# Performance work log

Measured on AMD Instinct MI355X. Metric: run time of the kernel, lower is better.

The kernel has to match this reference:

```python
import jax, jax.numpy as jnp
import numpy as np

C = 384
NUM_HEADS = 6
HEAD_SIZE = C // NUM_HEADS
EPS = 1e-5


def setup_inputs() -> dict:
    key = jax.random.key(0)
    ks = jax.random.split(key, 16)
    sc = lambda *s: 0.02
    inp = {
        'x': jax.random.normal(ks[0], (256, 256, C), dtype=jnp.float32),
        'Wq': jax.random.normal(ks[1], (NUM_HEADS, C, HEAD_SIZE), dtype=jnp.float32) * 0.02,
        'Wk': jax.random.normal(ks[2], (NUM_HEADS, C, HEAD_SIZE), dtype=jnp.float32) * 0.02,
        'Wv': jax.random.normal(ks[3], (NUM_HEADS, C, HEAD_SIZE), dtype=jnp.float32) * 0.02,
        'Wp': jax.random.normal(ks[4], (C, C), dtype=jnp.float32) * 0.02,
        'bp': jnp.zeros((C,), dtype=jnp.float32),
        'W1': jax.random.normal(ks[5], (C, 4 * C), dtype=jnp.float32) * 0.02,
        'b1': jnp.zeros((4 * C,), dtype=jnp.float32),
        'W2': jax.random.normal(ks[6], (4 * C, C), dtype=jnp.float32) * 0.02,
        'b2': jnp.zeros((C,), dtype=jnp.float32),
        'g1': jnp.ones((C,), dtype=jnp.float32),
        'be1': jnp.zeros((C,), dtype=jnp.float32),
        'g2': jnp.ones((C,), dtype=jnp.float32),
        'be2': jnp.zeros((C,), dtype=jnp.float32),
    }
    return inp


def _layernorm(x, g, b):
    mu = jnp.mean(x, axis=-1, keepdims=True)
    var = jnp.mean(jnp.square(x - mu), axis=-1, keepdims=True)
    return (x - mu) * jax.lax.rsqrt(var + EPS) * g + b


def reference(x, Wq, Wk, Wv, Wp, bp, W1, b1, W2, b2, g1, be1, g2, be2):
    B, T, _ = x.shape
    # --- attention sublayer (dropout = identity in eval) ---
    h = _layernorm(x, g1, be1)
    Q = jnp.einsum('btc,hcd->bhtd', h, Wq)
    K = jnp.einsum('btc,hcd->bhtd', h, Wk)
    V = jnp.einsum('btc,hcd->bhtd', h, Wv)
    scores = jnp.einsum('bhtd,bhsd->bhts', Q, K) / jnp.sqrt(jnp.float32(HEAD_SIZE))
    causal = jnp.tril(jnp.ones((T, T), dtype=bool))
    scores = jnp.where(causal, scores, -jnp.inf)
    attn = jax.nn.softmax(scores, axis=-1)
    out = jnp.einsum('bhts,bhsd->bhtd', attn, V)  # [B,H,T,d]
    out = out.transpose(0, 2, 1, 3).reshape(B, T, C)  # concat heads
    x = x + out @ Wp + bp
    # --- feed-forward sublayer ---
    h2 = _layernorm(x, g2, be2)
    ff = jax.nn.relu(h2 @ W1 + b1) @ W2 + b2
    return x + ff
```

## Files before the change

### kernel.cpp

```cpp
#include <hip/hip_runtime.h>
#include <hip/hip_bf16.h>


typedef __attribute__((ext_vector_type(8))) short bf16x8;
typedef __attribute__((ext_vector_type(4))) float f32x4;
typedef unsigned short u16;
typedef unsigned int u32;

#define MFMA16(a, b, c) __builtin_amdgcn_mfma_f32_16x16x32_bf16((a), (b), (c), 0, 0, 0)

__device__ __forceinline__ void gl2lds16(const void* g, void* l) {
  __builtin_amdgcn_global_load_lds((const __attribute__((address_space(1))) u32*)g,
                                   (__attribute__((address_space(3))) u32*)l, 16, 0, 0);
}

__device__ __forceinline__ u16 f2bf(float f) {
  __hip_bfloat16 h = __float2bfloat16(f);
  return *(u16*)&h;
}
__device__ __forceinline__ float bf2f(u16 u) {
  __hip_bfloat16 h;
  *(u16*)&h = u;
  return __bfloat162float(h);
}

template <int HAS_BIAS, int HAS_RES, int RELU, int OUT_BF16>
__global__ __launch_bounds__(256) void gemm_bt(const u16* __restrict__ A,
                                               const u16* __restrict__ Bt,
                                               const float* __restrict__ bias,
                                               const float* res, void* outp,
                                               int M, int N, int K) {
  __shared__ __attribute__((aligned(16))) u16 As[128 * 32];
  __shared__ __attribute__((aligned(16))) u16 Bs[128 * 32];
  const int m0 = blockIdx.y * 128, n0 = blockIdx.x * 128;
  const int w = threadIdx.x >> 6, l = threadIdx.x & 63;
  const int lm = l & 15, quad = l >> 4;
  const int wm = (w >> 1) * 64, wn = (w & 1) * 64;
  f32x4 acc[4][4];
#pragma unroll
  for (int i = 0; i < 4; ++i)
#pragma unroll
    for (int j = 0; j < 4; ++j) acc[i][j] = 0.f;

  for (int k0 = 0; k0 < K; k0 += 32) {
#pragma unroll
    for (int j = 0; j < 2; ++j) {
      int ci = w * 128 + j * 64 + l;
      int row = ci >> 2, cc = ci & 3;
      gl2lds16(A + (size_t)(m0 + row) * K + k0 + cc * 8, &As[(w * 128 + j * 64) * 8]);
      gl2lds16(Bt + (size_t)(n0 + row) * K + k0 + cc * 8, &Bs[(w * 128 + j * 64) * 8]);
    }
    __syncthreads();
    bf16x8 af[4], bfb[4];
#pragma unroll
    for (int i = 0; i < 4; ++i)
      af[i] = *(const bf16x8*)&As[(wm + i * 16 + lm) * 32 + quad * 8];
#pragma unroll
    for (int j = 0; j < 4; ++j)
      bfb[j] = *(const bf16x8*)&Bs[(wn + j * 16 + lm) * 32 + quad * 8];
#pragma unroll
    for (int i = 0; i < 4; ++i)
#pragma unroll
      for (int j = 0; j < 4; ++j) acc[i][j] = MFMA16(af[i], bfb[j], acc[i][j]);
    __syncthreads();
  }
#pragma unroll
  for (int i = 0; i < 4; ++i) {
#pragma unroll
    for (int j = 0; j < 4; ++j) {
      int col = n0 + wn + j * 16 + lm;
      float bs = HAS_BIAS ? bias[col] : 0.f;
#pragma unroll
      for (int r = 0; r < 4; ++r) {
        int row = m0 + wm + i * 16 + quad * 4 + r;
        float v = acc[i][j][r] + bs;
        if (RELU) v = fmaxf(v, 0.f);
        if (HAS_RES) v += res[(size_t)row * N + col];
        if (OUT_BF16)
          ((u16*)outp)[(size_t)row * N + col] = f2bf(v);
        else
          ((float*)outp)[(size_t)row * N + col] = v;
      }
    }
  }
}

__global__ __launch_bounds__(256) void ln_kernel(const float* __restrict__ x,
                                                 const float* __restrict__ g,
                                                 const float* __restrict__ be,
                                                 u16* __restrict__ out) {
  int row = blockIdx.x * 4 + (threadIdx.x >> 6);
  int l = threadIdx.x & 63;
  const float* xr = x + (size_t)row * 384;
  float v[6];
  float s = 0.f;
#pragma unroll
  for (int i = 0; i < 6; ++i) {
    v[i] = xr[l + i * 64];
    s += v[i];
  }
#pragma unroll
  for (int o = 1; o < 64; o <<= 1) s += __shfl_xor(s, o, 64);
  float mu = s * (1.f / 384.f);
  float var = 0.f;
#pragma unroll
  for (int i = 0; i < 6; ++i) {
    float d = v[i] - mu;
    var += d * d;
  }
#pragma unroll
  for (int o = 1; o < 64; o <<= 1) var += __shfl_xor(var, o, 64);
  float rs = rsqrtf(var * (1.f / 384.f) + 1e-5f);
  u16* orow = out + (size_t)row * 384;
#pragma unroll
  for (int i = 0; i < 6; ++i)
    orow[l + i * 64] = f2bf((v[i] - mu) * rs * g[l + i * 64] + be[l + i * 64]);
}

__global__ void wT_kernel(const float* __restrict__ in, u16* __restrict__ out,
                          int K, int N) {
  int idx = blockIdx.x * 256 + threadIdx.x;
  if (idx >= K * N) return;
  int n = idx / K, k = idx - n * K;
  out[idx] = f2bf(in[(size_t)k * N + n]);
}

__global__ void qkvT_kernel(const float* __restrict__ W, u16* __restrict__ out) {
  int idx = blockIdx.x * 256 + threadIdx.x;
  if (idx >= 6 * 384 * 64) return;
  int r = idx / 384;
  int c = idx - r * 384;
  int h = r >> 6, d = r & 63;
  out[idx] = f2bf(W[(size_t)(h * 384 + c) * 64 + d]);
}

template <int TQ>
__global__ __launch_bounds__(256) void attn_kernel(const u16* __restrict__ qkv,
                                                   u16* __restrict__ attnout) {
  constexpr int NFULL = (TQ + 1) * 64;
  constexpr int NJ = NFULL / 16;
  constexpr int KSTEPS = NFULL / 32;
  int bh = blockIdx.x;
  int h = bh % 6, b = bh / 6;
  int tid = threadIdx.x;
  int w = tid >> 6, l = tid & 63;
  int lm = l & 15, quad = l >> 4;

  __shared__ __attribute__((aligned(16))) unsigned char smx[65536];
  u16* Qs = (u16*)smx;
  u16* Ks = (u16*)(smx + 9216);
  u16* P = (u16*)smx;
  u16* Vt = (u16*)(smx + 32768);

  const u16* Qg = qkv + ((size_t)(b * 256 + TQ * 64)) * 1152 + h * 64;
  const u16* Kg = qkv + ((size_t)(b * 256)) * 1152 + 384 + h * 64;
  const u16* Vg = qkv + ((size_t)(b * 256)) * 1152 + 768 + h * 64;

  for (int i = tid; i < 64 * 64; i += 256) {
    int r = i >> 6, d = i & 63;
    Qs[r * 72 + d] = f2bf(0.125f * bf2f(Qg[(size_t)r * 1152 + d]));
  }
  for (int i = tid; i < NFULL * 64; i += 256) {
    int r = i >> 6, d = i & 63;
    Ks[r * 72 + d] = Kg[(size_t)r * 1152 + d];
  }
  __syncthreads();

  f32x4 sacc[NJ];
#pragma unroll
  for (int jt = 0; jt < NJ; ++jt) sacc[jt] = 0.f;
#pragma unroll
  for (int kk = 0; kk < 2; ++kk) {
    bf16x8 aq = *(const bf16x8*)&Qs[(w * 16 + lm) * 72 + kk * 32 + quad * 8];
#pragma unroll
    for (int jt = 0; jt < NJ; ++jt) {
      bf16x8 bk = *(const bf16x8*)&Ks[(jt * 16 + lm) * 72 + kk * 32 + quad * 8];
      sacc[jt] = MFMA16(aq, bk, sacc[jt]);
    }
  }
  __syncthreads();

  int trow = TQ * 64 + w * 16 + quad * 4;
  float inv_l[4];
#pragma unroll
  for (int reg = 0; reg < 4; ++reg) {
    float m_ = -3.0e38f;
#pragma unroll
    for (int jt = 0; jt < NJ; ++jt) {
      int col = jt * 16 + lm;
      if (col <= trow + reg) m_ = fmaxf(m_, sacc[jt][reg]);
    }
#pragma unroll
    for (int o = 1; o < 16; o <<= 1) m_ = fmaxf(m_, __shfl_xor(m_, o, 16));
    float s_ = 0.f;
#pragma unroll
    for (int jt = 0; jt < NJ; ++jt) {
      int col = jt * 16 + lm;
      float p = (col <= trow + reg) ? __expf(sacc[jt][reg] - m_) : 0.f;
      sacc[jt][reg] = p;
      s_ += p;
    }
#pragma unroll
    for (int o = 1; o < 16; o <<= 1) s_ += __shfl_xor(s_, o, 16);
    inv_l[reg] = 1.f / s_;
  }
#pragma unroll
  for (int jt = 0; jt < NJ; ++jt) {
#pragma unroll
    for (int reg = 0; reg < 4; ++reg) {
      int m = w * 16 + quad * 4 + reg;
      int col = jt * 16 + lm;
      P[m * 256 + (col ^ ((m & 7) * 8))] = f2bf(sacc[jt][reg] * inv_l[reg]);
    }
  }
  for (int i = tid; i < NFULL * 64; i += 256) {
    int s = i >> 6, d = i & 63;
    Vt[d * 256 + (s ^ ((d & 7) * 8))] = Vg[(size_t)s * 1152 + d];
  }
  __syncthreads();

  f32x4 oacc[4];
#pragma unroll
  for (int jt = 0; jt < 4; ++jt) oacc[jt] = 0.f;
#pragma unroll
  for (int ks = 0; ks < KSTEPS; ++ks) {
    int m = w * 16 + lm;
    int kc = ks * 32 + quad * 8;
    bf16x8 ap = *(const bf16x8*)&P[m * 256 + (kc ^ ((m & 7) * 8))];
#pragma unroll
    for (int jt = 0; jt < 4; ++jt) {
      int n = jt * 16 + lm;
      bf16x8 bv = *(const bf16x8*)&Vt[n * 256 + (kc ^ ((n & 7) * 8))];
      oacc[jt] = MFMA16(ap, bv, oacc[jt]);
    }
  }
  u16* Og = attnout + ((size_t)(b * 256 + TQ * 64)) * 384 + h * 64;
#pragma unroll
  for (int jt = 0; jt < 4; ++jt)
#pragma unroll
    for (int r = 0; r < 4; ++r)
      Og[(size_t)(w * 16 + quad * 4 + r) * 384 + jt * 16 + lm] = f2bf(oacc[jt][r]);
}

extern "C" void kernel_launch(void* const* d_in, const int* in_sizes, int n_in,
                              void* d_out, int out_size, void* d_ws, size_t ws_size,
                              hipStream_t stream) {
  const float* x = (const float*)d_in[0];
  const float* Wq = (const float*)d_in[1];
  const float* Wk = (const float*)d_in[2];
  const float* Wv = (const float*)d_in[3];
  const float* Wp = (const float*)d_in[4];
  const float* bp = (const float*)d_in[5];
  const float* W1 = (const float*)d_in[6];
  const float* b1 = (const float*)d_in[7];
  const float* W2 = (const float*)d_in[8];
  const float* b2 = (const float*)d_in[9];
  const float* g1 = (const float*)d_in[10];
  const float* be1 = (const float*)d_in[11];
  const float* g2 = (const float*)d_in[12];
  const float* be2 = (const float*)d_in[13];
  float* out = (float*)d_out;

  const int BT = 65536;
  char* ws = (char*)d_ws;
  u16* qkv = (u16*)(ws);
  u16* attnout = (u16*)(ws + 150994944);
  u16* ff1 = (u16*)(ws);
  u16* h = (u16*)(ws + 201326592);
  u16* WqkvT = (u16*)(ws + 251658240);
  u16* WpT = (u16*)(ws + 252542976);
  u16* W1T = (u16*)(ws + 252837888);
  u16* W2T = (u16*)(ws + 254017536);

  qkvT_kernel<<<576, 256, 0, stream>>>(Wq, WqkvT);
  qkvT_kernel<<<576, 256, 0, stream>>>(Wk, WqkvT + 384 * 384);
  qkvT_kernel<<<576, 256, 0, stream>>>(Wv, WqkvT + 2 * 384 * 384);
  wT_kernel<<<576, 256, 0, stream>>>(Wp, WpT, 384, 384);
  wT_kernel<<<2304, 256, 0, stream>>>(W1, W1T, 384, 1536);
  wT_kernel<<<2304, 256, 0, stream>>>(W2, W2T, 1536, 384);

  ln_kernel<<<BT / 4, 256, 0, stream>>>(x, g1, be1, h);
  gemm_bt<0, 0, 0, 1><<<dim3(9, 512), 256, 0, stream>>>(h, WqkvT, nullptr, nullptr,
                                                        qkv, BT, 1152, 384);
  attn_kernel<0><<<1536, 256, 0, stream>>>(qkv, attnout);
  attn_kernel<1><<<1536, 256, 0, stream>>>(qkv, attnout);
  attn_kernel<2><<<1536, 256, 0, stream>>>(qkv, attnout);
  attn_kernel<3><<<1536, 256, 0, stream>>>(qkv, attnout);
  gemm_bt<1, 1, 0, 0><<<dim3(3, 512), 256, 0, stream>>>(attnout, WpT, bp, x, out,
                                                        BT, 384, 384);
  ln_kernel<<<BT / 4, 256, 0, stream>>>(out, g2, be2, h);
  gemm_bt<1, 0, 1, 1><<<dim3(12, 512), 256, 0, stream>>>(h, W1T, b1, nullptr, ff1,
                                                         BT, 1536, 384);
  gemm_bt<1, 1, 0, 0><<<dim3(3, 512), 256, 0, stream>>>(ff1, W2T, b2, out, out,
                                                        BT, 384, 1536);
}
```

Baseline: 905.9 us.

## Widen GEMM K-tile with swizzle, head-major QKV layout, fuse attention launches

The GEMM loads 64-wide K tiles into XOR-swizzled LDS and remaps block IDs so neighbouring M tiles stay on one XCD. The QKV projection writes a head-major layout, so attention can load Q, K and V with 16-byte vector loads. The Q scaling is folded into the softmax exponent, and the four attention launches become one grid. LayerNorm uses float2 loads and packed bf16 stores. The cost is larger LDS use per GEMM block and a scattered store pattern in the QKV epilogue.

```diff
diff --git a/kernel.cpp b/kernel.cpp
--- a/kernel.cpp
+++ b/kernel.cpp
@@ -23,16 +23,23 @@
   *(u16*)&h = u;
   return __bfloat162float(h);
 }
-
-template <int HAS_BIAS, int HAS_RES, int RELU, int OUT_BF16>
+__device__ __forceinline__ u32 pack2(float lo, float hi) {
+  return (u32)f2bf(lo) | ((u32)f2bf(hi) << 16);
+}
+
+template <int HAS_BIAS, int HAS_RES, int RELU, int OUT_MODE>
 __global__ __launch_bounds__(256) void gemm_bt(const u16* __restrict__ A,
                                                const u16* __restrict__ Bt,
                                                const float* __restrict__ bias,
                                                const float* res, void* outp,
-                                               int M, int N, int K) {
-  __shared__ __attribute__((aligned(16))) u16 As[128 * 32];
-  __shared__ __attribute__((aligned(16))) u16 Bs[128 * 32];
-  const int m0 = blockIdx.y * 128, n0 = blockIdx.x * 128;
+                                               int M, int N, int K, int gx) {
+  __shared__ __attribute__((aligned(16))) u16 As[128 * 64];
+  __shared__ __attribute__((aligned(16))) u16 Bs[128 * 64];
+  const int bid = blockIdx.x;
+  const int s = bid >> 3, xcd = bid & 7;
+  const int gy8 = gridDim.x / (8 * gx);
+  const int nI = s % gx, mC = s / gx;
+  const int m0 = (xcd * gy8 + mC) * 128, n0 = nI * 128;
   const int w = threadIdx.x >> 6, l = threadIdx.x & 63;
   const int lm = l & 15, quad = l >> 4;
   const int wm = (w >> 1) * 64, wn = (w & 1) * 64;
@@ -42,26 +49,35 @@
 #pragma unroll
     for (int j = 0; j < 4; ++j) acc[i][j] = 0.f;
 
-  for (int k0 = 0; k0 < K; k0 += 32) {
-#pragma unroll
-    for (int j = 0; j < 2; ++j) {
-      int ci = w * 128 + j * 64 + l;
-      int row = ci >> 2, cc = ci & 3;
-      gl2lds16(A + (size_t)(m0 + row) * K + k0 + cc * 8, &As[(w * 128 + j * 64) * 8]);
-      gl2lds16(Bt + (size_t)(n0 + row) * K + k0 + cc * 8, &Bs[(w * 128 + j * 64) * 8]);
+  for (int k0 = 0; k0 < K; k0 += 64) {
+#pragma unroll
+    for (int j = 0; j < 4; ++j) {
+      int ell = (w * 4 + j) * 64 + l;
+      int row = ell >> 3;
+      int cs = ell & 7;
+      int cg = cs ^ (row & 7);
+      gl2lds16(A + (size_t)(m0 + row) * K + k0 + cg * 8, &As[(w * 4 + j) * 64 * 8]);
+      gl2lds16(Bt + (size_t)(n0 + row) * K + k0 + cg * 8, &Bs[(w * 4 + j) * 64 * 8]);
     }
     __syncthreads();
-    bf16x8 af[4], bfb[4];
-#pragma unroll
-    for (int i = 0; i < 4; ++i)
-      af[i] = *(const bf16x8*)&As[(wm + i * 16 + lm) * 32 + quad * 8];
-#pragma unroll
-    for (int j = 0; j < 4; ++j)
-      bfb[j] = *(const bf16x8*)&Bs[(wn + j * 16 + lm) * 32 + quad * 8];
-#pragma unroll
-    for (int i = 0; i < 4; ++i)
-#pragma unroll
-      for (int j = 0; j < 4; ++j) acc[i][j] = MFMA16(af[i], bfb[j], acc[i][j]);
+#pragma unroll
+    for (int ks = 0; ks < 2; ++ks) {
+      bf16x8 af[4], bfb[4];
+#pragma unroll
+      for (int i = 0; i < 4; ++i) {
+        int r = wm + i * 16 + lm;
+        af[i] = *(const bf16x8*)&As[r * 64 + (((ks * 4 + quad) ^ (r & 7)) * 8)];
+      }
+#pragma unroll
+      for (int j = 0; j < 4; ++j) {
+        int r = wn + j * 16 + lm;
+        bfb[j] = *(const bf16x8*)&Bs[r * 64 + (((ks * 4 + quad) ^ (r & 7)) * 8)];
+      }
+#pragma unroll
+      for (int i = 0; i < 4; ++i)
+#pragma unroll
+        for (int j = 0; j < 4; ++j) acc[i][j] = MFMA16(af[i], bfb[j], acc[i][j]);
+    }
     __syncthreads();
   }
 #pragma unroll
@@ -76,10 +92,16 @@
         float v = acc[i][j][r] + bs;
         if (RELU) v = fmaxf(v, 0.f);
         if (HAS_RES) v += res[(size_t)row * N + col];
-        if (OUT_BF16)
+        if (OUT_MODE == 0) {
+          ((float*)outp)[(size_t)row * N + col] = v;
+        } else if (OUT_MODE == 1) {
           ((u16*)outp)[(size_t)row * N + col] = f2bf(v);
-        else
-          ((float*)outp)[(size_t)row * N + col] = v;
+        } else {
+          int sel = col / 384;
+          int rem = col - sel * 384;
+          int hh = rem >> 6, dd = rem & 63;
+          ((u16*)outp)[((size_t)(sel * 6 + hh) * 65536 + row) * 64 + dd] = f2bf(v);
+        }
       }
     }
   }
@@ -91,14 +113,12 @@
                                                  u16* __restrict__ out) {
   int row = blockIdx.x * 4 + (threadIdx.x >> 6);
   int l = threadIdx.x & 63;
-  const float* xr = x + (size_t)row * 384;
-  float v[6];
+  const float2* xr = (const float2*)(x + (size_t)row * 384 + l * 6);
+  float2 t0 = xr[0], t1 = xr[1], t2 = xr[2];
+  float v[6] = {t0.x, t0.y, t1.x, t1.y, t2.x, t2.y};
   float s = 0.f;
 #pragma unroll
-  for (int i = 0; i < 6; ++i) {
-    v[i] = xr[l + i * 64];
-    s += v[i];
-  }
+  for (int i = 0; i < 6; ++i) s += v[i];
 #pragma unroll
   for (int o = 1; o < 64; o <<= 1) s += __shfl_xor(s, o, 64);
   float mu = s * (1.f / 384.f);
@@ -111,10 +131,19 @@
 #pragma unroll
   for (int o = 1; o < 64; o <<= 1) var += __shfl_xor(var, o, 64);
   float rs = rsqrtf(var * (1.f / 384.f) + 1e-5f);
-  u16* orow = out + (size_t)row * 384;
-#pragma unroll
-  for (int i = 0; i < 6; ++i)
-    orow[l + i * 64] = f2bf((v[i] - mu) * rs * g[l + i * 64] + be[l + i * 64]);
+  const float2* gg = (const float2*)(g + l * 6);
+  const float2* bb = (const float2*)(be + l * 6);
+  float2 g0 = gg[0], g1 = gg[1], g2 = gg[2];
+  float2 b0 = bb[0], b1 = bb[1], b2 = bb[2];
+  float gv[6] = {g0.x, g0.y, g1.x, g1.y, g2.x, g2.y};
+  float bv[6] = {b0.x, b0.y, b1.x, b1.y, b2.x, b2.y};
+  float o_[6];
+#pragma unroll
+  for (int i = 0; i < 6; ++i) o_[i] = (v[i] - mu) * rs * gv[i] + bv[i];
+  u32* orow = (u32*)(out + (size_t)row * 384 + l * 6);
+  orow[0] = pack2(o_[0], o_[1]);
+  orow[1] = pack2(o_[2], o_[3]);
+  orow[2] = pack2(o_[4], o_[5]);
 }
 
 __global__ void wT_kernel(const float* __restrict__ in, u16* __restrict__ out,
@@ -135,34 +164,34 @@
 }
 
 template <int TQ>
-__global__ __launch_bounds__(256) void attn_kernel(const u16* __restrict__ qkv,
-                                                   u16* __restrict__ attnout) {
+__device__ __forceinline__ void attn_body(const u16* __restrict__ qkv,
+                                          u16* __restrict__ attnout,
+                                          unsigned char* smx) {
   constexpr int NFULL = (TQ + 1) * 64;
   constexpr int NJ = NFULL / 16;
   constexpr int KSTEPS = NFULL / 32;
-  int bh = blockIdx.x;
+  int bh = blockIdx.y;
   int h = bh % 6, b = bh / 6;
   int tid = threadIdx.x;
   int w = tid >> 6, l = tid & 63;
   int lm = l & 15, quad = l >> 4;
 
-  __shared__ __attribute__((aligned(16))) unsigned char smx[65536];
   u16* Qs = (u16*)smx;
   u16* Ks = (u16*)(smx + 9216);
   u16* P = (u16*)smx;
   u16* Vt = (u16*)(smx + 32768);
 
-  const u16* Qg = qkv + ((size_t)(b * 256 + TQ * 64)) * 1152 + h * 64;
-  const u16* Kg = qkv + ((size_t)(b * 256)) * 1152 + 384 + h * 64;
-  const u16* Vg = qkv + ((size_t)(b * 256)) * 1152 + 768 + h * 64;
-
-  for (int i = tid; i < 64 * 64; i += 256) {
-    int r = i >> 6, d = i & 63;
-    Qs[r * 72 + d] = f2bf(0.125f * bf2f(Qg[(size_t)r * 1152 + d]));
-  }
-  for (int i = tid; i < NFULL * 64; i += 256) {
-    int r = i >> 6, d = i & 63;
-    Ks[r * 72 + d] = Kg[(size_t)r * 1152 + d];
+  const u16* Qg = qkv + ((size_t)h * 65536 + b * 256 + TQ * 64) * 64;
+  const u16* Kg = qkv + ((size_t)(6 + h) * 65536 + b * 256) * 64;
+  const u16* Vg = qkv + ((size_t)(12 + h) * 65536 + b * 256) * 64;
+
+  for (int i = tid; i < 64 * 8; i += 256) {
+    int r = i >> 3, cs = i & 7;
+    *(bf16x8*)&Qs[r * 72 + cs * 8] = *(const bf16x8*)&Qg[r * 64 + cs * 8];
+  }
+  for (int i = tid; i < NFULL * 8; i += 256) {
+    int r = i >> 3, cs = i & 7;
+    *(bf16x8*)&Ks[r * 72 + cs * 8] = *(const bf16x8*)&Kg[r * 64 + cs * 8];
   }
   __syncthreads();
 
@@ -196,7 +225,7 @@
 #pragma unroll
     for (int jt = 0; jt < NJ; ++jt) {
       int col = jt * 16 + lm;
-      float p = (col <= trow + reg) ? __expf(sacc[jt][reg] - m_) : 0.f;
+      float p = (col <= trow + reg) ? __expf(0.125f * (sacc[jt][reg] - m_)) : 0.f;
       sacc[jt][reg] = p;
       s_ += p;
     }
@@ -213,9 +242,14 @@
       P[m * 256 + (col ^ ((m & 7) * 8))] = f2bf(sacc[jt][reg] * inv_l[reg]);
     }
   }
-  for (int i = tid; i < NFULL * 64; i += 256) {
-    int s = i >> 6, d = i & 63;
-    Vt[d * 256 + (s ^ ((d & 7) * 8))] = Vg[(size_t)s * 1152 + d];
+  for (int i = tid; i < NFULL * 8; i += 256) {
+    int sr = i >> 3, cs = i & 7;
+    bf16x8 vv = *(const bf16x8*)&Vg[sr * 64 + cs * 8];
+#pragma unroll
+    for (int j = 0; j < 8; ++j) {
+      int d = cs * 8 + j;
+      Vt[d * 256 + (sr ^ ((d & 7) * 8))] = (u16)vv[j];
+    }
   }
   __syncthreads();
 
@@ -240,6 +274,17 @@
 #pragma unroll
     for (int r = 0; r < 4; ++r)
       Og[(size_t)(w * 16 + quad * 4 + r) * 384 + jt * 16 + lm] = f2bf(oacc[jt][r]);
+}
+
+__global__ __launch_bounds__(256) void attn_all(const u16* __restrict__ qkv,
+                                                u16* __restrict__ attnout) {
+  __shared__ __attribute__((aligned(16))) unsigned char smx[65536];
+  switch (blockIdx.x) {
+    case 0: attn_body<0>(qkv, attnout, smx); break;
+    case 1: attn_body<1>(qkv, attnout, smx); break;
+    case 2: attn_body<2>(qkv, attnout, smx); break;
+    default: attn_body<3>(qkv, attnout, smx); break;
+  }
 }
 
 extern "C" void kernel_launch(void* const* d_in, const int* in_sizes, int n_in,
@@ -280,17 +325,14 @@
   wT_kernel<<<2304, 256, 0, stream>>>(W2, W2T, 1536, 384);
 
   ln_kernel<<<BT / 4, 256, 0, stream>>>(x, g1, be1, h);
-  gemm_bt<0, 0, 0, 1><<<dim3(9, 512), 256, 0, stream>>>(h, WqkvT, nullptr, nullptr,
-                                                        qkv, BT, 1152, 384);
-  attn_kernel<0><<<1536, 256, 0, stream>>>(qkv, attnout);
-  attn_kernel<1><<<1536, 256, 0, stream>>>(qkv, attnout);
-  attn_kernel<2><<<1536, 256, 0, stream>>>(qkv, attnout);
-  attn_kernel<3><<<1536, 256, 0, stream>>>(qkv, attnout);
-  gemm_bt<1, 1, 0, 0><<<dim3(3, 512), 256, 0, stream>>>(attnout, WpT, bp, x, out,
-                                                        BT, 384, 384);
+  gemm_bt<0, 0, 0, 2><<<9 * 512, 256, 0, stream>>>(h, WqkvT, nullptr, nullptr,
+                                                   qkv, BT, 1152, 384, 9);
+  attn_all<<<dim3(4, 1536), 256, 0, stream>>>(qkv, attnout);
+  gemm_bt<1, 1, 0, 0><<<3 * 512, 256, 0, stream>>>(attnout, WpT, bp, x, out,
+                                                   BT, 384, 384, 3);
   ln_kernel<<<BT / 4, 256, 0, stream>>>(out, g2, be2, h);
-  gemm_bt<1, 0, 1, 1><<<dim3(12, 512), 256, 0, stream>>>(h, W1T, b1, nullptr, ff1,
-                                                         BT, 1536, 384);
-  gemm_bt<1, 1, 0, 0><<<dim3(3, 512), 256, 0, stream>>>(ff1, W2T, b2, out, out,
-                                                        BT, 384, 1536);
-}
+  gemm_bt<1, 0, 1, 1><<<12 * 512, 256, 0, stream>>>(h, W1T, b1, nullptr, ff1,
+                                                    BT, 1536, 384, 12);
+  gemm_bt<1, 1, 0, 0><<<3 * 512, 256, 0, stream>>>(ff1, W2T, b2, out, out,
+                                                   BT, 384, 1536, 3);
+}
```

Result: faster. 811.2 us (-10.5%).
